# Kernel tuning notes

Hardware: AMD Instinct MI355X
Metric: run time of the kernel (lower is better)

## Reference

```python
import jax, jax.numpy as jnp
import numpy as np

EPS = 1e-5

def _weight_quant(w):
    # BitNet b1.58: per-tensor ternary quantization with STE.
    scale = 1.0 / jnp.maximum(jnp.mean(jnp.abs(w)), EPS)
    wq = jnp.clip(jnp.round(w * scale), -1.0, 1.0) / scale
    return w + jax.lax.stop_gradient(wq - w)

def _act_quant(x):
    # per-token int8 absmax quantization with STE.
    scale = 127.0 / jnp.maximum(jnp.max(jnp.abs(x), axis=-1, keepdims=True), EPS)
    xq = jnp.clip(jnp.round(x * scale), -128.0, 127.0) / scale
    return x + jax.lax.stop_gradient(xq - x)

def _bitlinear(x, w):
    # x: [..., in], w: [out, in] (torch layout)
    return jnp.einsum('bsd,hd->bsh', _act_quant(x), _weight_quant(w))

def setup_inputs() -> dict:
    key = jax.random.key(0)
    k1, k2, k3, k4 = jax.random.split(key, 4)
    B, S, D, H = 4, 2048, 2048, 5632
    x = jax.random.normal(k1, (B, S, D), dtype=jnp.float32)
    w1 = jax.random.normal(k2, (H, D), dtype=jnp.float32) * 0.02
    w2 = jax.random.normal(k3, (H, D), dtype=jnp.float32) * 0.02
    w3 = jax.random.normal(k4, (D, H), dtype=jnp.float32) * 0.02
    return {"x": x, "w1": w1, "w2": w2, "w3": w3}

def reference(x, w1, w2, w3):
    gate = jax.nn.silu(_bitlinear(x, w1))   # [B,S,H]
    up = _bitlinear(x, w2)                  # [B,S,H]
    h = gate * up                           # [B,S,H]
    return _bitlinear(h, w3)                # [B,S,D]
```

## Files before the change

kernel.cpp:

```cpp
#include <hip/hip_runtime.h>
#include <hip/hip_bf16.h>
#include <math.h>

#define EPSQ 1e-5f

typedef __attribute__((ext_vector_type(4))) int i32x4;

__device__ __forceinline__ void gload_lds16(const void* g, void* l) {
  __builtin_amdgcn_global_load_lds(
      (__attribute__((address_space(1))) void*)g,
      (__attribute__((address_space(3))) void*)l, 16, 0, 0);
}

__device__ __forceinline__ int clampi8(float v, float lo, float hi) {
  return (int)rintf(fminf(hi, fmaxf(lo, v)));
}

__global__ void wabs3_kernel(const float* __restrict__ w1, const float* __restrict__ w2,
                             const float* __restrict__ w3, int n4,
                             double* __restrict__ sums) {
  const float* w = (blockIdx.y == 0) ? w1 : (blockIdx.y == 1) ? w2 : w3;
  __shared__ double sm[256];
  const float4* w4 = (const float4*)w;
  double acc = 0.0;
  const int stride = gridDim.x * blockDim.x;
  for (int i = blockIdx.x * blockDim.x + threadIdx.x; i < n4; i += stride) {
    float4 v = w4[i];
    acc += (double)fabsf(v.x) + (double)fabsf(v.y) + (double)fabsf(v.z) + (double)fabsf(v.w);
  }
  sm[threadIdx.x] = acc;
  __syncthreads();
  for (int s = 128; s > 0; s >>= 1) {
    if ((int)threadIdx.x < s) sm[threadIdx.x] += sm[threadIdx.x + s];
    __syncthreads();
  }
  if (threadIdx.x == 0) atomicAdd(sums + blockIdx.y, sm[0]);
}

__global__ void wquant3_kernel(const float* __restrict__ w1, const float* __restrict__ w2,
                               const float* __restrict__ w3, int n4,
                               const double* __restrict__ sums, double inv_n,
                               unsigned int* __restrict__ q1, unsigned int* __restrict__ q2,
                               unsigned int* __restrict__ q3) {
  const int wsel = blockIdx.y;
  const float* w = (wsel == 0) ? w1 : (wsel == 1) ? w2 : w3;
  unsigned int* wq = (wsel == 0) ? q1 : (wsel == 1) ? q2 : q3;
  const float s = (float)fmax(sums[wsel] * inv_n, (double)EPSQ);
  const float scale = 1.0f / s;
  const int i = blockIdx.x * blockDim.x + threadIdx.x;
  if (i >= n4) return;
  float4 v = ((const float4*)w)[i];
  const int b0 = clampi8(rintf(v.x * scale), -1.f, 1.f);
  const int b1 = clampi8(rintf(v.y * scale), -1.f, 1.f);
  const int b2 = clampi8(rintf(v.z * scale), -1.f, 1.f);
  const int b3 = clampi8(rintf(v.w * scale), -1.f, 1.f);
  wq[i] = (unsigned int)((b0 & 0xff) | ((b1 & 0xff) << 8) |
                         ((b2 & 0xff) << 16) | ((b3 & 0xff) << 24));
}

__global__ void aquant_kernel(const float* __restrict__ x, int K,
                              unsigned char* __restrict__ q, float* __restrict__ arow) {
  const int row = blockIdx.x;
  const int n4 = K >> 2;
  const float4* xr = (const float4*)(x + (size_t)row * K);
  float m = 0.f;
  for (int c = threadIdx.x; c < n4; c += blockDim.x) {
    float4 v = xr[c];
    m = fmaxf(m, fmaxf(fmaxf(fabsf(v.x), fabsf(v.y)), fmaxf(fabsf(v.z), fabsf(v.w))));
  }
  __shared__ float sm[256];
  sm[threadIdx.x] = m;
  __syncthreads();
  for (int s = 128; s > 0; s >>= 1) {
    if ((int)threadIdx.x < s) sm[threadIdx.x] = fmaxf(sm[threadIdx.x], sm[threadIdx.x + s]);
    __syncthreads();
  }
  const float mv = fmaxf(sm[0], EPSQ);
  const float scale = 127.0f / mv;
  if (threadIdx.x == 0) arow[row] = mv * (1.0f / 127.0f);
  unsigned int* qr = (unsigned int*)(q + (size_t)row * K);
  for (int c = threadIdx.x; c < n4; c += blockDim.x) {
    float4 v = xr[c];
    const int b0 = clampi8(v.x * scale, -128.f, 127.f);
    const int b1 = clampi8(v.y * scale, -128.f, 127.f);
    const int b2 = clampi8(v.z * scale, -128.f, 127.f);
    const int b3 = clampi8(v.w * scale, -128.f, 127.f);
    qr[c] = (unsigned int)((b0 & 0xff) | ((b1 & 0xff) << 8) |
                           ((b2 & 0xff) << 16) | ((b3 & 0xff) << 24));
  }
}

__global__ void aquant_pre_kernel(const float* __restrict__ x, int K,
                                  const float* __restrict__ hpart, int nslice,
                                  unsigned char* __restrict__ q, float* __restrict__ arow) {
  const int row = blockIdx.x;
  __shared__ float sm[256];
  float m = 0.f;
  for (int t = threadIdx.x; t < nslice; t += blockDim.x)
    m = fmaxf(m, hpart[(size_t)row * nslice + t]);
  sm[threadIdx.x] = m;
  __syncthreads();
  for (int s = 128; s > 0; s >>= 1) {
    if ((int)threadIdx.x < s) sm[threadIdx.x] = fmaxf(sm[threadIdx.x], sm[threadIdx.x + s]);
    __syncthreads();
  }
  const float mv = fmaxf(sm[0], EPSQ);
  const float scale = 127.0f / mv;
  if (threadIdx.x == 0) arow[row] = mv * (1.0f / 127.0f);
  const int n4 = K >> 2;
  const float4* xr = (const float4*)(x + (size_t)row * K);
  unsigned int* qr = (unsigned int*)(q + (size_t)row * K);
  for (int c = threadIdx.x; c < n4; c += blockDim.x) {
    float4 v = xr[c];
    const int b0 = clampi8(v.x * scale, -128.f, 127.f);
    const int b1 = clampi8(v.y * scale, -128.f, 127.f);
    const int b2 = clampi8(v.z * scale, -128.f, 127.f);
    const int b3 = clampi8(v.w * scale, -128.f, 127.f);
    qr[c] = (unsigned int)((b0 & 0xff) | ((b1 & 0xff) << 8) |
                           ((b2 & 0xff) << 16) | ((b3 & 0xff) << 24));
  }
}

#define BKP 64

#define PIPE_BARRIER(N)                                         \
  asm volatile("s_waitcnt vmcnt(" #N ")" ::: "memory");         \
  __builtin_amdgcn_s_barrier();                                 \
  asm volatile("" ::: "memory");

#define GU_SLOT 32768

__launch_bounds__(512, 2)
__global__ void gemm_gateup(const unsigned char* __restrict__ Aq,
                            const unsigned char* __restrict__ W1q,
                            const unsigned char* __restrict__ W2q,
                            const float* __restrict__ arow,
                            const double* __restrict__ wsum,
                            float* __restrict__ Hbuf,
                            float* __restrict__ hpart,
                            const int N, const int K,
                            const int MBb, const int NBb) {
  __shared__ char lds[3 * GU_SLOT];

  const int tid = threadIdx.x;
  const int lane = tid & 63;
  const int wid = tid >> 6;
  const int wm = wid >> 1;
  const int wn = wid & 1;

  const int total = MBb * NBb;
  int swz = blockIdx.x;
  if ((total & 7) == 0) swz = (swz & 7) * (total >> 3) + (swz >> 3);
  const int nb = swz % NBb;
  const int mb = swz / NBb;
  const int m0 = mb * 256;
  const int n0 = nb * 128;

  const unsigned char* Ab  = Aq  + (size_t)m0 * K;
  const unsigned char* B1b = W1q + (size_t)n0 * K;
  const unsigned char* B2b = W2q + (size_t)n0 * K;

  auto stage = [&](int kt, int s) {
    const int k0 = kt * BKP;
    char* base = lds + s * GU_SLOT;
#pragma unroll
    for (int is = 0; is < 2; ++is) {
      const int p = is * 8192 + wid * 1024 + lane * 16;
      const int r = p >> 6;
      const int c = ((p >> 4) & 3) ^ ((r >> 1) & 3);
      gload_lds16(Ab + (size_t)r * K + k0 + c * 16, base + is * 8192 + wid * 1024);
    }
    {
      const int p = wid * 1024 + lane * 16;
      const int r = p >> 6;
      const int c = ((p >> 4) & 3) ^ ((r >> 1) & 3);
      const size_t go = (size_t)r * K + k0 + c * 16;
      gload_lds16(B1b + go, base + 16384 + wid * 1024);
      gload_lds16(B2b + go, base + 24576 + wid * 1024);
    }
  };

  const int c16 = lane >> 4;
  int offA[4], offB1[4], offB2[4];
#pragma unroll
  for (int i = 0; i < 4; ++i) {
    const int row = wm * 64 + i * 16 + (lane & 15);
    offA[i] = row * 64 + ((c16 ^ ((row >> 1) & 3)) << 4);
  }
#pragma unroll
  for (int j = 0; j < 4; ++j) {
    const int n = wn * 64 + j * 16 + (lane & 15);
    const int o = n * 64 + ((c16 ^ ((n >> 1) & 3)) << 4);
    offB1[j] = 16384 + o;
    offB2[j] = 24576 + o;
  }

  i32x4 acc1[4][4] = {};
  i32x4 acc2[4][4] = {};

  const int NT = K / BKP;
  stage(0, 0);
  stage(1, 1);
  PIPE_BARRIER(4)

  int s = 0, s2 = 2;
  for (int t = 0; t < NT; ++t) {
    if (t + 2 < NT) stage(t + 2, s2);
    const char* sb = lds + s * GU_SLOT;
    i32x4 af[4], b1f[4], b2f[4];
#pragma unroll
    for (int i = 0; i < 4; ++i) af[i] = *(const i32x4*)(sb + offA[i]);
#pragma unroll
    for (int j = 0; j < 4; ++j) {
      b1f[j] = *(const i32x4*)(sb + offB1[j]);
      b2f[j] = *(const i32x4*)(sb + offB2[j]);
    }
    __builtin_amdgcn_s_setprio(1);
#pragma unroll
    for (int j = 0; j < 4; ++j)
#pragma unroll
      for (int i = 0; i < 4; ++i) {
        acc1[i][j] = __builtin_amdgcn_mfma_i32_16x16x64_i8(af[i], b1f[j], acc1[i][j], 0, 0, 0);
        acc2[i][j] = __builtin_amdgcn_mfma_i32_16x16x64_i8(af[i], b2f[j], acc2[i][j], 0, 0, 0);
      }
    __builtin_amdgcn_s_setprio(0);
    if (t + 2 < NT) {
      PIPE_BARRIER(4)
    } else if (t + 1 < NT) {
      PIPE_BARRIER(0)
    }
    s = (s == 2) ? 0 : s + 1;
    s2 = (s2 == 2) ? 0 : s2 + 1;
  }

  const double inv_n = 1.0 / 11534336.0;
  const float sw1 = (float)fmax(wsum[0] * inv_n, (double)EPSQ);
  const float sw2 = (float)fmax(wsum[1] * inv_n, (double)EPSQ);
  const int nslice = NBb * 2;
  const int slice = nb * 2 + wn;
#pragma unroll
  for (int i = 0; i < 4; ++i) {
    const int rb = m0 + wm * 64 + i * 16 + (lane >> 4) * 4;
#pragma unroll
    for (int qe = 0; qe < 4; ++qe) {
      const int grow = rb + qe;
      const float a = arow[grow];
      const float f1 = a * sw1;
      const float f2 = a * sw2;
      float* hr = Hbuf + (size_t)grow * N + n0 + wn * 64 + (lane & 15);
      float lmax = 0.f;
#pragma unroll
      for (int j = 0; j < 4; ++j) {
        const float y1 = (float)acc1[i][j][qe] * f1;
        const float y2 = (float)acc2[i][j][qe] * f2;
        const float h = (y1 / (1.0f + expf(-y1))) * y2;
        hr[j * 16] = h;
        lmax = fmaxf(lmax, fabsf(h));
      }
#pragma unroll
      for (int mk = 8; mk >= 1; mk >>= 1)
        lmax = fmaxf(lmax, __shfl_xor(lmax, mk, 64));
      if ((lane & 15) == 0)
        hpart[(size_t)grow * nslice + slice] = lmax;
    }
  }
}

#define DN_SLOT 24576

__launch_bounds__(512, 2)
__global__ void gemm_down(const unsigned char* __restrict__ Aq,
                          const unsigned char* __restrict__ Wq,
                          const float* __restrict__ arow,
                          const double* __restrict__ wsum,
                          float* __restrict__ Out,
                          const int N, const int K,
                          const int MBb, const int NBb) {
  __shared__ char lds[3 * DN_SLOT];

  const int tid = threadIdx.x;
  const int lane = tid & 63;
  const int wid = tid >> 6;
  const int wm = wid >> 1;
  const int wn = wid & 1;

  const int total = MBb * NBb;
  int swz = blockIdx.x;
  if ((total & 7) == 0) swz = (swz & 7) * (total >> 3) + (swz >> 3);
  const int nb = swz % NBb;
  const int mb = swz / NBb;
  const int m0 = mb * 256;
  const int n0 = nb * 128;

  const unsigned char* Ab = Aq + (size_t)m0 * K;
  const unsigned char* Bb = Wq + (size_t)n0 * K;

  auto stage = [&](int kt, int s) {
    const int k0 = kt * BKP;
    char* base = lds + s * DN_SLOT;
#pragma unroll
    for (int is = 0; is < 2; ++is) {
      const int p = is * 8192 + wid * 1024 + lane * 16;
      const int r = p >> 6;
      const int c = ((p >> 4) & 3) ^ ((r >> 1) & 3);
      gload_lds16(Ab + (size_t)r * K + k0 + c * 16, base + is * 8192 + wid * 1024);
    }
    {
      const int p = wid * 1024 + lane * 16;
      const int r = p >> 6;
      const int c = ((p >> 4) & 3) ^ ((r >> 1) & 3);
      gload_lds16(Bb + (size_t)r * K + k0 + c * 16, base + 16384 + wid * 1024);
    }
  };

  const int c16 = lane >> 4;
  int offA[4], offB[4];
#pragma unroll
  for (int i = 0; i < 4; ++i) {
    const int row = wm * 64 + i * 16 + (lane & 15);
    offA[i] = row * 64 + ((c16 ^ ((row >> 1) & 3)) << 4);
  }
#pragma unroll
  for (int j = 0; j < 4; ++j) {
    const int n = wn * 64 + j * 16 + (lane & 15);
    offB[j] = 16384 + n * 64 + ((c16 ^ ((n >> 1) & 3)) << 4);
  }

  i32x4 acc[4][4] = {};

  const int NT = K / BKP;
  stage(0, 0);
  stage(1, 1);
  PIPE_BARRIER(3)

  int s = 0, s2 = 2;
  for (int t = 0; t < NT; ++t) {
    if (t + 2 < NT) stage(t + 2, s2);
    const char* sb = lds + s * DN_SLOT;
    i32x4 af[4], bf[4];
#pragma unroll
    for (int i = 0; i < 4; ++i) af[i] = *(const i32x4*)(sb + offA[i]);
#pragma unroll
    for (int j = 0; j < 4; ++j) bf[j] = *(const i32x4*)(sb + offB[j]);
    __builtin_amdgcn_s_setprio(1);
#pragma unroll
    for (int j = 0; j < 4; ++j)
#pragma unroll
      for (int i = 0; i < 4; ++i)
        acc[i][j] = __builtin_amdgcn_mfma_i32_16x16x64_i8(af[i], bf[j], acc[i][j], 0, 0, 0);
    __builtin_amdgcn_s_setprio(0);
    if (t + 2 < NT) {
      PIPE_BARRIER(3)
    } else if (t + 1 < NT) {
      PIPE_BARRIER(0)
    }
    s = (s == 2) ? 0 : s + 1;
    s2 = (s2 == 2) ? 0 : s2 + 1;
  }

  const double inv_n = 1.0 / 11534336.0;
  const float sw3 = (float)fmax(wsum[2] * inv_n, (double)EPSQ);
#pragma unroll
  for (int i = 0; i < 4; ++i) {
    const int rb = m0 + wm * 64 + i * 16 + (lane >> 4) * 4;
#pragma unroll
    for (int qe = 0; qe < 4; ++qe) {
      const int grow = rb + qe;
      const float f = arow[grow] * sw3;
      float* orow = Out + (size_t)grow * N + n0 + wn * 64 + (lane & 15);
#pragma unroll
      for (int j = 0; j < 4; ++j) {
        orow[j * 16] = (float)acc[i][j][qe] * f;
      }
    }
  }
}

extern "C" void kernel_launch(void* const* d_in, const int* in_sizes, int n_in,
                              void* d_out, int out_size, void* d_ws, size_t ws_size,
                              hipStream_t stream) {
  (void)n_in; (void)out_size;
  const float* x  = (const float*)d_in[0];
  const float* w1 = (const float*)d_in[1];
  const float* w2 = (const float*)d_in[2];
  const float* w3 = (const float*)d_in[3];
  float* out = (float*)d_out;

  const int D = 2048, H = 5632;
  const int M = in_sizes[0] / D;
  const long long NW = (long long)H * D;
  const int NBgu = H / 128;
  const int NBdn = D / 128;
  const int nslice = NBgu * 2;

  auto al = [](size_t v) { return (v + 255) & ~(size_t)255; };

  size_t off = 0;
  const size_t o_wsum = off; off += al(3 * sizeof(double));
  const size_t o_w1q  = off; off += al((size_t)NW);
  const size_t o_w2q  = off; off += al((size_t)NW);
  const size_t o_w3q  = off; off += al((size_t)NW);
  const size_t fixed = off;

  int Mc = 256;
  for (int cand = M; cand >= 256; cand >>= 1) {
    size_t need = fixed
                + al((size_t)cand * 4)
                + al((size_t)cand * 4)
                + al((size_t)cand * nslice * 4)
                + al((size_t)cand * D)
                + al((size_t)cand * H * 4)
                + al((size_t)cand * H);
    if (need <= ws_size) { Mc = cand; break; }
  }

  size_t coff = fixed;
  const size_t o_arow1 = coff; coff += al((size_t)Mc * 4);
  const size_t o_arow2 = coff; coff += al((size_t)Mc * 4);
  const size_t o_hpart = coff; coff += al((size_t)Mc * nslice * 4);
  const size_t o_qx    = coff; coff += al((size_t)Mc * D);
  const size_t o_hbuf  = coff; coff += al((size_t)Mc * H * 4);
  const size_t o_qh    = coff; coff += al((size_t)Mc * H);

  char* ws = (char*)d_ws;
  double* wsum        = (double*)(ws + o_wsum);
  unsigned char* w1q  = (unsigned char*)(ws + o_w1q);
  unsigned char* w2q  = (unsigned char*)(ws + o_w2q);
  unsigned char* w3q  = (unsigned char*)(ws + o_w3q);
  float* arow1        = (float*)(ws + o_arow1);
  float* arow2        = (float*)(ws + o_arow2);
  float* hpart        = (float*)(ws + o_hpart);
  unsigned char* qx   = (unsigned char*)(ws + o_qx);
  float* hbuf         = (float*)(ws + o_hbuf);
  unsigned char* qh   = (unsigned char*)(ws + o_qh);

  hipMemsetAsync(wsum, 0, 3 * sizeof(double), stream);

  const int n4w = (int)(NW / 4);
  wabs3_kernel<<<dim3(1024, 3), 256, 0, stream>>>(w1, w2, w3, n4w, wsum);

  const double inv_n = 1.0 / (double)NW;
  wquant3_kernel<<<dim3(n4w / 256, 3), 256, 0, stream>>>(
      w1, w2, w3, n4w, wsum, inv_n,
      (unsigned int*)w1q, (unsigned int*)w2q, (unsigned int*)w3q);

  for (int c = 0; c < M; c += Mc) {
    const int MBb = Mc / 256;
    aquant_kernel<<<Mc, 256, 0, stream>>>(x + (size_t)c * D, D, qx, arow1);
    gemm_gateup<<<MBb * NBgu, 512, 0, stream>>>(qx, w1q, w2q, arow1, wsum,
                                                hbuf, hpart, H, D, MBb, NBgu);
    aquant_pre_kernel<<<Mc, 256, 0, stream>>>(hbuf, H, hpart, nslice, qh, arow2);
    gemm_down<<<MBb * NBdn, 512, 0, stream>>>(qh, w3q, arow2, wsum,
                                              out + (size_t)c * D, D, H, MBb, NBdn);
  }
}
```

Baseline: 485.7 us.

## Interleave LDS reads, global prefetch and MFMA in phased ping-pong schedule

Both int8 GEMM main loops are split into sub-phases. Each phase issues a slice of the LDS fragment reads and one part of the next-tile global->LDS prefetch, then waits at a block barrier (with lgkmcnt(0) and a sched_barrier) before a burst of MFMAs. The goal is to spread memory issue across the MFMA work and coordinate waves so compute and loads alternate. The cost is several extra s_barriers per K-step, which can stall waves and reduce the overlap the compiler already achieved.

```diff
diff --git a/kernel.cpp b/kernel.cpp
--- a/kernel.cpp
+++ b/kernel.cpp
@@ -128,6 +128,16 @@
   __builtin_amdgcn_s_barrier();                                 \
   asm volatile("" ::: "memory");
 
+#define PRE_MFMA_FENCE()                                        \
+  asm volatile("" ::: "memory");                                \
+  __builtin_amdgcn_s_barrier();                                 \
+  asm volatile("s_waitcnt lgkmcnt(0)" ::: "memory");            \
+  __builtin_amdgcn_sched_barrier(0);
+
+#define POST_MFMA_FENCE()                                       \
+  __builtin_amdgcn_s_barrier();                                 \
+  asm volatile("" ::: "memory");
+
 #define GU_SLOT 32768
 
 __launch_bounds__(512, 2)
@@ -160,23 +170,24 @@
   const unsigned char* B1b = W1q + (size_t)n0 * K;
   const unsigned char* B2b = W2q + (size_t)n0 * K;
 
-  auto stage = [&](int kt, int s) {
+  const int p0 = wid * 1024 + lane * 16;
+  const int r0 = p0 >> 6;
+  const int cb0 = ((p0 >> 4) & 3) ^ ((r0 >> 1) & 3);
+  const int p1 = 8192 + p0;
+  const int r1 = p1 >> 6;
+  const int cb1 = ((p1 >> 4) & 3) ^ ((r1 >> 1) & 3);
+
+  auto stage_part = [&](int kt, int s, int q) {
     const int k0 = kt * BKP;
     char* base = lds + s * GU_SLOT;
-#pragma unroll
-    for (int is = 0; is < 2; ++is) {
-      const int p = is * 8192 + wid * 1024 + lane * 16;
-      const int r = p >> 6;
-      const int c = ((p >> 4) & 3) ^ ((r >> 1) & 3);
-      gload_lds16(Ab + (size_t)r * K + k0 + c * 16, base + is * 8192 + wid * 1024);
-    }
-    {
-      const int p = wid * 1024 + lane * 16;
-      const int r = p >> 6;
-      const int c = ((p >> 4) & 3) ^ ((r >> 1) & 3);
-      const size_t go = (size_t)r * K + k0 + c * 16;
-      gload_lds16(B1b + go, base + 16384 + wid * 1024);
-      gload_lds16(B2b + go, base + 24576 + wid * 1024);
+    if (q == 0) {
+      gload_lds16(Ab + (size_t)r0 * K + k0 + cb0 * 16, base + wid * 1024);
+    } else if (q == 1) {
+      gload_lds16(Ab + (size_t)r1 * K + k0 + cb1 * 16, base + 8192 + wid * 1024);
+    } else if (q == 2) {
+      gload_lds16(B1b + (size_t)r0 * K + k0 + cb0 * 16, base + 16384 + wid * 1024);
+    } else {
+      gload_lds16(B2b + (size_t)r0 * K + k0 + cb0 * 16, base + 24576 + wid * 1024);
     }
   };
 
@@ -199,32 +210,40 @@
   i32x4 acc2[4][4] = {};
 
   const int NT = K / BKP;
-  stage(0, 0);
-  stage(1, 1);
+#pragma unroll
+  for (int q = 0; q < 4; ++q) stage_part(0, 0, q);
+#pragma unroll
+  for (int q = 0; q < 4; ++q) stage_part(1, 1, q);
   PIPE_BARRIER(4)
 
   int s = 0, s2 = 2;
   for (int t = 0; t < NT; ++t) {
-    if (t + 2 < NT) stage(t + 2, s2);
+    const bool pf = (t + 2 < NT);
     const char* sb = lds + s * GU_SLOT;
-    i32x4 af[4], b1f[4], b2f[4];
-#pragma unroll
-    for (int i = 0; i < 4; ++i) af[i] = *(const i32x4*)(sb + offA[i]);
-#pragma unroll
-    for (int j = 0; j < 4; ++j) {
-      b1f[j] = *(const i32x4*)(sb + offB1[j]);
-      b2f[j] = *(const i32x4*)(sb + offB2[j]);
-    }
-    __builtin_amdgcn_s_setprio(1);
-#pragma unroll
-    for (int j = 0; j < 4; ++j)
-#pragma unroll
-      for (int i = 0; i < 4; ++i) {
-        acc1[i][j] = __builtin_amdgcn_mfma_i32_16x16x64_i8(af[i], b1f[j], acc1[i][j], 0, 0, 0);
-        acc2[i][j] = __builtin_amdgcn_mfma_i32_16x16x64_i8(af[i], b2f[j], acc2[i][j], 0, 0, 0);
-      }
-    __builtin_amdgcn_s_setprio(0);
-    if (t + 2 < NT) {
+#pragma unroll
+    for (int q = 0; q < 4; ++q) {
+      const int qi = q >> 1, qj = q & 1;
+      i32x4 a0  = *(const i32x4*)(sb + offA[2 * qi]);
+      i32x4 a1  = *(const i32x4*)(sb + offA[2 * qi + 1]);
+      i32x4 b1a = *(const i32x4*)(sb + offB1[2 * qj]);
+      i32x4 b1b = *(const i32x4*)(sb + offB1[2 * qj + 1]);
+      i32x4 b2a = *(const i32x4*)(sb + offB2[2 * qj]);
+      i32x4 b2b = *(const i32x4*)(sb + offB2[2 * qj + 1]);
+      if (pf) stage_part(t + 2, s2, q);
+      PRE_MFMA_FENCE()
+      __builtin_amdgcn_s_setprio(1);
+      acc1[2*qi][2*qj]     = __builtin_amdgcn_mfma_i32_16x16x64_i8(a0, b1a, acc1[2*qi][2*qj], 0, 0, 0);
+      acc1[2*qi][2*qj+1]   = __builtin_amdgcn_mfma_i32_16x16x64_i8(a0, b1b, acc1[2*qi][2*qj+1], 0, 0, 0);
+      acc1[2*qi+1][2*qj]   = __builtin_amdgcn_mfma_i32_16x16x64_i8(a1, b1a, acc1[2*qi+1][2*qj], 0, 0, 0);
+      acc1[2*qi+1][2*qj+1] = __builtin_amdgcn_mfma_i32_16x16x64_i8(a1, b1b, acc1[2*qi+1][2*qj+1], 0, 0, 0);
+      acc2[2*qi][2*qj]     = __builtin_amdgcn_mfma_i32_16x16x64_i8(a0, b2a, acc2[2*qi][2*qj], 0, 0, 0);
+      acc2[2*qi][2*qj+1]   = __builtin_amdgcn_mfma_i32_16x16x64_i8(a0, b2b, acc2[2*qi][2*qj+1], 0, 0, 0);
+      acc2[2*qi+1][2*qj]   = __builtin_amdgcn_mfma_i32_16x16x64_i8(a1, b2a, acc2[2*qi+1][2*qj], 0, 0, 0);
+      acc2[2*qi+1][2*qj+1] = __builtin_amdgcn_mfma_i32_16x16x64_i8(a1, b2b, acc2[2*qi+1][2*qj+1], 0, 0, 0);
+      __builtin_amdgcn_s_setprio(0);
+      if (q < 3) { POST_MFMA_FENCE() }
+    }
+    if (pf) {
       PIPE_BARRIER(4)
     } else if (t + 1 < NT) {
       PIPE_BARRIER(0)
@@ -295,21 +314,22 @@
   const unsigned char* Ab = Aq + (size_t)m0 * K;
   const unsigned char* Bb = Wq + (size_t)n0 * K;
 
-  auto stage = [&](int kt, int s) {
+  const int p0 = wid * 1024 + lane * 16;
+  const int r0 = p0 >> 6;
+  const int cb0 = ((p0 >> 4) & 3) ^ ((r0 >> 1) & 3);
+  const int p1 = 8192 + p0;
+  const int r1 = p1 >> 6;
+  const int cb1 = ((p1 >> 4) & 3) ^ ((r1 >> 1) & 3);
+
+  auto stage_part = [&](int kt, int s, int q) {
     const int k0 = kt * BKP;
     char* base = lds + s * DN_SLOT;
-#pragma unroll
-    for (int is = 0; is < 2; ++is) {
-      const int p = is * 8192 + wid * 1024 + lane * 16;
-      const int r = p >> 6;
-      const int c = ((p >> 4) & 3) ^ ((r >> 1) & 3);
-      gload_lds16(Ab + (size_t)r * K + k0 + c * 16, base + is * 8192 + wid * 1024);
-    }
-    {
-      const int p = wid * 1024 + lane * 16;
-      const int r = p >> 6;
-      const int c = ((p >> 4) & 3) ^ ((r >> 1) & 3);
-      gload_lds16(Bb + (size_t)r * K + k0 + c * 16, base + 16384 + wid * 1024);
+    if (q == 0) {
+      gload_lds16(Ab + (size_t)r0 * K + k0 + cb0 * 16, base + wid * 1024);
+    } else if (q == 1) {
+      gload_lds16(Ab + (size_t)r1 * K + k0 + cb1 * 16, base + 8192 + wid * 1024);
+    } else {
+      gload_lds16(Bb + (size_t)r0 * K + k0 + cb0 * 16, base + 16384 + wid * 1024);
     }
   };
 
@@ -329,27 +349,50 @@
   i32x4 acc[4][4] = {};
 
   const int NT = K / BKP;
-  stage(0, 0);
-  stage(1, 1);
+#pragma unroll
+  for (int q = 0; q < 3; ++q) stage_part(0, 0, q);
+#pragma unroll
+  for (int q = 0; q < 3; ++q) stage_part(1, 1, q);
   PIPE_BARRIER(3)
 
   int s = 0, s2 = 2;
   for (int t = 0; t < NT; ++t) {
-    if (t + 2 < NT) stage(t + 2, s2);
+    const bool pf = (t + 2 < NT);
     const char* sb = lds + s * DN_SLOT;
-    i32x4 af[4], bf[4];
-#pragma unroll
-    for (int i = 0; i < 4; ++i) af[i] = *(const i32x4*)(sb + offA[i]);
-#pragma unroll
-    for (int j = 0; j < 4; ++j) bf[j] = *(const i32x4*)(sb + offB[j]);
+    i32x4 af0 = *(const i32x4*)(sb + offA[0]);
+    i32x4 af1 = *(const i32x4*)(sb + offA[1]);
+    i32x4 af2 = *(const i32x4*)(sb + offA[2]);
+    i32x4 af3 = *(const i32x4*)(sb + offA[3]);
+    i32x4 bf0 = *(const i32x4*)(sb + offB[0]);
+    i32x4 bf1 = *(const i32x4*)(sb + offB[1]);
+    if (pf) { stage_part(t + 2, s2, 0); stage_part(t + 2, s2, 1); }
+    PRE_MFMA_FENCE()
     __builtin_amdgcn_s_setprio(1);
-#pragma unroll
-    for (int j = 0; j < 4; ++j)
-#pragma unroll
-      for (int i = 0; i < 4; ++i)
-        acc[i][j] = __builtin_amdgcn_mfma_i32_16x16x64_i8(af[i], bf[j], acc[i][j], 0, 0, 0);
+    acc[0][0] = __builtin_amdgcn_mfma_i32_16x16x64_i8(af0, bf0, acc[0][0], 0, 0, 0);
+    acc[1][0] = __builtin_amdgcn_mfma_i32_16x16x64_i8(af1, bf0, acc[1][0], 0, 0, 0);
+    acc[2][0] = __builtin_amdgcn_mfma_i32_16x16x64_i8(af2, bf0, acc[2][0], 0, 0, 0);
+    acc[3][0] = __builtin_amdgcn_mfma_i32_16x16x64_i8(af3, bf0, acc[3][0], 0, 0, 0);
+    acc[0][1] = __builtin_amdgcn_mfma_i32_16x16x64_i8(af0, bf1, acc[0][1], 0, 0, 0);
+    acc[1][1] = __builtin_amdgcn_mfma_i32_16x16x64_i8(af1, bf1, acc[1][1], 0, 0, 0);
+    acc[2][1] = __builtin_amdgcn_mfma_i32_16x16x64_i8(af2, bf1, acc[2][1], 0, 0, 0);
+    acc[3][1] = __builtin_amdgcn_mfma_i32_16x16x64_i8(af3, bf1, acc[3][1], 0, 0, 0);
     __builtin_amdgcn_s_setprio(0);
-    if (t + 2 < NT) {
+    POST_MFMA_FENCE()
+    i32x4 bf2 = *(const i32x4*)(sb + offB[2]);
+    i32x4 bf3 = *(const i32x4*)(sb + offB[3]);
+    if (pf) stage_part(t + 2, s2, 2);
+    PRE_MFMA_FENCE()
+    __builtin_amdgcn_s_setprio(1);
+    acc[0][2] = __builtin_amdgcn_mfma_i32_16x16x64_i8(af0, bf2, acc[0][2], 0, 0, 0);
+    acc[1][2] = __builtin_amdgcn_mfma_i32_16x16x64_i8(af1, bf2, acc[1][2], 0, 0, 0);
+    acc[2][2] = __builtin_amdgcn_mfma_i32_16x16x64_i8(af2, bf2, acc[2][2], 0, 0, 0);
+    acc[3][2] = __builtin_amdgcn_mfma_i32_16x16x64_i8(af3, bf2, acc[3][2], 0, 0, 0);
+    acc[0][3] = __builtin_amdgcn_mfma_i32_16x16x64_i8(af0, bf3, acc[0][3], 0, 0, 0);
+    acc[1][3] = __builtin_amdgcn_mfma_i32_16x16x64_i8(af1, bf3, acc[1][3], 0, 0, 0);
+    acc[2][3] = __builtin_amdgcn_mfma_i32_16x16x64_i8(af2, bf3, acc[2][3], 0, 0, 0);
+    acc[3][3] = __builtin_amdgcn_mfma_i32_16x16x64_i8(af3, bf3, acc[3][3], 0, 0, 0);
+    __builtin_amdgcn_s_setprio(0);
+    if (pf) {
       PIPE_BARRIER(3)
     } else if (t + 1 < NT) {
       PIPE_BARRIER(0)
```

New measurement: 524.9 us. 8.1% more time.
